# Kernel tuning notes

Measured on AMD Instinct MI355X. Metric: run time of the kernel, lower is better.

The kernel has to match this reference:

```python
import jax, jax.numpy as jnp
import numpy as np


def smooth_l1(x, y):
    d = jnp.abs(x - y)
    return jnp.where(d < 1.0, 0.5 * d * d, d - 0.5)


def setup_inputs() -> dict:
    key = jax.random.key(0)
    k1, k2, k3 = jax.random.split(key, 3)
    B, T, N, D = 4, 28, 1024, 3
    X_v = jax.random.normal(k1, (B, T, N, D), dtype=jnp.float32)
    target_X_v = jax.random.normal(k2, (B, T, N, D), dtype=jnp.float32)
    weights = jax.random.uniform(k3, (B, T), dtype=jnp.float32)
    return {"X_v": X_v, "target_X_v": target_X_v, "weights": weights}


def reference(X_v, target_X_v, weights):
    B = X_v.shape[0]
    # Pairwise squared distances [B,T,N,N] via ||p||^2 + ||t||^2 - 2 p.t
    pn = jnp.sum(X_v * X_v, axis=-1)                 # [B,T,N]
    tn = jnp.sum(target_X_v * target_X_v, axis=-1)   # [B,T,N]
    dist = (pn[..., :, None] + tn[..., None, :]
            - 2.0 * jnp.einsum('btnd,btmd->btnm', X_v, target_X_v))
    minv = jnp.argmin(dist, axis=-1)                 # [B,T,N] int
    # gather nearest target point for each pred point
    tagp = jnp.take_along_axis(target_X_v, minv[..., None], axis=2)  # [B,T,N,3]
    # per-(b,t) mean smooth-L1 over N points x 3 coords
    loss_bt = jnp.mean(smooth_l1(X_v, tagp), axis=(-2, -1))          # [B,T]
    loss = jnp.sum(loss_bt * weights) / B

    prec = jnp.mean(X_v, axis=2)        # [B,T,3]
    tarc = jnp.mean(target_X_v, axis=2) # [B,T,3]
    lossc = jnp.sum(smooth_l1(prec, tarc)) / (B * 3)
    return (loss, lossc)
```

## Files before the change

### kernel.cpp

```cpp
#include <hip/hip_runtime.h>

constexpr int Bc = 4;
constexpr int Tc = 28;
constexpr int Nc = 1024;
constexpr int Dc = 3;
constexpr int BT = Bc * Tc;
constexpr int QT = 256;
constexpr int NQ = 4;

constexpr size_t WS_BESTV = 0;
constexpr size_t WS_BESTI = (size_t)NQ * BT * 256 * 4;
constexpr size_t WS_PSUM  = WS_BESTI + (size_t)NQ * BT * 256 * 4;
constexpr size_t WS_TSUM  = WS_PSUM + BT * 3;

__device__ __forceinline__ float sl1(float d) {
    d = fabsf(d);
    return d < 1.0f ? 0.5f * d * d : d - 0.5f;
}

__global__ __launch_bounds__(256) void chamfer_kernel(
    const float* __restrict__ X, const float* __restrict__ Tg,
    float4* __restrict__ bestvP, int4* __restrict__ bestiP,
    float* __restrict__ psum, float* __restrict__ tsum)
{
    __shared__ float4 sT4[QT];
    __shared__ float sred[4][3];

    const int bt  = blockIdx.x >> 2;
    const int th  = blockIdx.x & 3;
    const int tid = threadIdx.x;

    const float4* x4 = (const float4*)(X + (size_t)bt * (Nc * Dc));
    const float4 a0 = x4[3 * tid + 0];
    const float4 a1 = x4[3 * tid + 1];
    const float4 a2 = x4[3 * tid + 2];

    if (tid < 64) {
        const float4* tg4 = (const float4*)(Tg + (size_t)bt * (Nc * Dc) + th * (QT * 3));
        const float4 r0 = tg4[3 * tid + 0];
        const float4 r1 = tg4[3 * tid + 1];
        const float4 r2 = tg4[3 * tid + 2];
        sT4[4 * tid + 0] = make_float4(r0.x, r0.y, r0.z, fmaf(r0.x, r0.x, fmaf(r0.y, r0.y, r0.z * r0.z)));
        sT4[4 * tid + 1] = make_float4(r0.w, r1.x, r1.y, fmaf(r0.w, r0.w, fmaf(r1.x, r1.x, r1.y * r1.y)));
        sT4[4 * tid + 2] = make_float4(r1.z, r1.w, r2.x, fmaf(r1.z, r1.z, fmaf(r1.w, r1.w, r2.x * r2.x)));
        sT4[4 * tid + 3] = make_float4(r2.y, r2.z, r2.w, fmaf(r2.y, r2.y, fmaf(r2.z, r2.z, r2.w * r2.w)));
        float tx = r0.x + r0.w + r1.z + r2.y;
        float ty = r0.y + r1.x + r1.w + r2.z;
        float tz = r0.z + r1.y + r2.x + r2.w;
        #pragma unroll
        for (int off = 32; off; off >>= 1) {
            tx += __shfl_down(tx, off, 64);
            ty += __shfl_down(ty, off, 64);
            tz += __shfl_down(tz, off, 64);
        }
        if (tid == 0) {
            tsum[(bt * NQ + th) * 3 + 0] = tx;
            tsum[(bt * NQ + th) * 3 + 1] = ty;
            tsum[(bt * NQ + th) * 3 + 2] = tz;
        }
    }
    __syncthreads();

    const float c0[4] = {-2.f * a0.x, -2.f * a0.w, -2.f * a1.z, -2.f * a2.y};
    const float c1[4] = {-2.f * a0.y, -2.f * a1.x, -2.f * a1.w, -2.f * a2.z};
    const float c2[4] = {-2.f * a0.z, -2.f * a1.y, -2.f * a2.x, -2.f * a2.w};

    float best[4] = {3.4e38f, 3.4e38f, 3.4e38f, 3.4e38f};
    int idx[4] = {0, 0, 0, 0};

    constexpr int PF = 4;
    float4 bufA[PF], bufB[PF];
    #pragma unroll
    for (int j = 0; j < PF; ++j) bufA[j] = sT4[j];

    for (int m0 = 0; m0 < QT; m0 += 2 * PF) {
        #pragma unroll
        for (int j = 0; j < PF; ++j) bufB[j] = sT4[m0 + PF + j];
        #pragma unroll
        for (int j = 0; j < PF; ++j) {
            const float4 t = bufA[j];
            const int m = m0 + j;
            #pragma unroll
            for (int k = 0; k < 4; ++k) {
                float v = fmaf(c0[k], t.x, fmaf(c1[k], t.y, fmaf(c2[k], t.z, t.w)));
                bool c = v < best[k]; best[k] = c ? v : best[k]; idx[k] = c ? m : idx[k];
            }
        }
        #pragma unroll
        for (int j = 0; j < PF; ++j) bufA[j] = sT4[(m0 + 2 * PF + j) & (QT - 1)];
        #pragma unroll
        for (int j = 0; j < PF; ++j) {
            const float4 t = bufB[j];
            const int m = m0 + PF + j;
            #pragma unroll
            for (int k = 0; k < 4; ++k) {
                float v = fmaf(c0[k], t.x, fmaf(c1[k], t.y, fmaf(c2[k], t.z, t.w)));
                bool c = v < best[k]; best[k] = c ? v : best[k]; idx[k] = c ? m : idx[k];
            }
        }
    }

    const size_t ob = ((size_t)th * BT + bt) * 256 + tid;
    bestvP[ob] = make_float4(best[0], best[1], best[2], best[3]);
    bestiP[ob] = make_int4(th * QT + idx[0], th * QT + idx[1],
                           th * QT + idx[2], th * QT + idx[3]);

    if (th == 0) {
        float sx = a0.x + a0.w + a1.z + a2.y;
        float sy = a0.y + a1.x + a1.w + a2.z;
        float sz = a0.z + a1.y + a2.x + a2.w;
        const int lane = tid & 63, wid = tid >> 6;
        #pragma unroll
        for (int off = 32; off; off >>= 1) {
            sx += __shfl_down(sx, off, 64);
            sy += __shfl_down(sy, off, 64);
            sz += __shfl_down(sz, off, 64);
        }
        if (lane == 0) { sred[wid][0] = sx; sred[wid][1] = sy; sred[wid][2] = sz; }
        __syncthreads();
        if (tid == 0) {
            #pragma unroll
            for (int k = 0; k < 3; ++k)
                psum[bt * 3 + k] = sred[0][k] + sred[1][k] + sred[2][k] + sred[3][k];
        }
    }
}

__global__ __launch_bounds__(256) void gather_finalize_kernel(
    const float* __restrict__ X, const float* __restrict__ Tg,
    const float* __restrict__ W,
    const float4* __restrict__ bestvP, const int4* __restrict__ bestiP,
    const float* __restrict__ psum, const float* __restrict__ tsum,
    float* __restrict__ out)
{
    __shared__ float sred[4];
    __shared__ float sred2[4];
    const int bt  = blockIdx.x;
    const int tid = threadIdx.x;
    const size_t rb = (size_t)bt * 256 + tid;

    float4 bv = bestvP[rb];
    int4   bi = bestiP[rb];
    float best[4] = {bv.x, bv.y, bv.z, bv.w};
    int   idx[4]  = {bi.x, bi.y, bi.z, bi.w};
    #pragma unroll
    for (int q = 1; q < NQ; ++q) {
        const float4 v2 = bestvP[(size_t)q * BT * 256 + rb];
        const int4   i2 = bestiP[(size_t)q * BT * 256 + rb];
        if (v2.x < best[0]) { best[0] = v2.x; idx[0] = i2.x; }
        if (v2.y < best[1]) { best[1] = v2.y; idx[1] = i2.y; }
        if (v2.z < best[2]) { best[2] = v2.z; idx[2] = i2.z; }
        if (v2.w < best[3]) { best[3] = v2.w; idx[3] = i2.w; }
    }

    const float* tb = Tg + (size_t)bt * (Nc * Dc);
    const float4* x4 = (const float4*)(X + (size_t)bt * (Nc * Dc));
    const float4 a0 = x4[3 * tid + 0];
    const float4 a1 = x4[3 * tid + 1];
    const float4 a2 = x4[3 * tid + 2];
    const float px[4] = {a0.x, a0.w, a1.z, a2.y};
    const float py[4] = {a0.y, a1.x, a1.w, a2.z};
    const float pz[4] = {a0.z, a1.y, a2.x, a2.w};

    float s = 0.0f;
    #pragma unroll
    for (int k = 0; k < 4; ++k) {
        const float tx = tb[idx[k] * 3 + 0];
        const float ty = tb[idx[k] * 3 + 1];
        const float tz = tb[idx[k] * 3 + 2];
        s += sl1(px[k] - tx) + sl1(py[k] - ty) + sl1(pz[k] - tz);
    }

    const int lane = tid & 63, wid = tid >> 6;
    #pragma unroll
    for (int off = 32; off; off >>= 1) s += __shfl_down(s, off, 64);
    if (lane == 0) sred[wid] = s;
    __syncthreads();
    if (tid == 0) {
        float tot = sred[0] + sred[1] + sred[2] + sred[3];
        atomicAdd(out, tot * W[bt] * (1.0f / (Nc * Dc)) * (1.0f / Bc));
    }

    if (bt == 0) {
        float lc = 0.0f;
        if (tid < BT) {
            const float inv = 1.0f / Nc;
            #pragma unroll
            for (int c = 0; c < 3; ++c) {
                float pm = psum[tid * 3 + c] * inv;
                float tm = (tsum[(tid * NQ + 0) * 3 + c] + tsum[(tid * NQ + 1) * 3 + c]
                          + tsum[(tid * NQ + 2) * 3 + c] + tsum[(tid * NQ + 3) * 3 + c]) * inv;
                lc += sl1(pm - tm);
            }
        }
        float v = lc;
        #pragma unroll
        for (int off = 32; off; off >>= 1) v += __shfl_down(v, off, 64);
        if (lane == 0) sred2[wid] = v;
        __syncthreads();
        if (tid == 0) {
            float tlc = sred2[0] + sred2[1] + sred2[2] + sred2[3];
            atomicAdd(out + 1, tlc * (1.0f / (Bc * Dc)));
        }
    }
}

extern "C" void kernel_launch(void* const* d_in, const int* in_sizes, int n_in,
                              void* d_out, int out_size, void* d_ws, size_t ws_size,
                              hipStream_t stream) {
    const float* X  = (const float*)d_in[0];
    const float* Tg = (const float*)d_in[1];
    const float* W  = (const float*)d_in[2];
    float* out = (float*)d_out;
    float* ws  = (float*)d_ws;

    float4* bestvP = (float4*)(ws + WS_BESTV);
    int4*   bestiP = (int4*)(ws + WS_BESTI);
    float*  psum   = ws + WS_PSUM;
    float*  tsum   = ws + WS_TSUM;

    hipMemsetAsync(out, 0, 2 * sizeof(float), stream);
    chamfer_kernel<<<BT * NQ, 256, 0, stream>>>(X, Tg, bestvP, bestiP, psum, tsum);
    gather_finalize_kernel<<<BT, 256, 0, stream>>>(X, Tg, W, bestvP, bestiP, psum, tsum, out);
}
```

Measured before the change: 85.61 us.

## Split targets into 8 chunks, read targets via uniform global loads, move centroid sums

Each (b,t) now has its target set split into 8 chunks of 128 instead of 4 of 256, giving 896 blocks for better CU fill. Target points are read directly from global memory with wave-uniform (scalar-friendly) loads, and their squared norm is recomputed in-loop instead of being staged through shared memory, which removes the LDS fill and the barrier. The centroid sums move into the finalize kernel, which now does a 7-value block reduction and applies the per-bt centroid loss with an atomic. In exchange, the finalize kernel reads twice as many partial results, and each inner step does a few extra FMAs for the norm.

```diff
diff --git a/kernel.cpp b/kernel.cpp
--- a/kernel.cpp
+++ b/kernel.cpp
@@ -5,136 +5,75 @@
 constexpr int Nc = 1024;
 constexpr int Dc = 3;
 constexpr int BT = Bc * Tc;
-constexpr int QT = 256;
-constexpr int NQ = 4;
+constexpr int TQ = 128;
+constexpr int NQ = Nc / TQ;
 
 constexpr size_t WS_BESTV = 0;
 constexpr size_t WS_BESTI = (size_t)NQ * BT * 256 * 4;
-constexpr size_t WS_PSUM  = WS_BESTI + (size_t)NQ * BT * 256 * 4;
-constexpr size_t WS_TSUM  = WS_PSUM + BT * 3;
 
 __device__ __forceinline__ float sl1(float d) {
     d = fabsf(d);
     return d < 1.0f ? 0.5f * d * d : d - 0.5f;
 }
 
-__global__ __launch_bounds__(256) void chamfer_kernel(
+__global__ __launch_bounds__(256, 4) void chamfer_kernel(
     const float* __restrict__ X, const float* __restrict__ Tg,
-    float4* __restrict__ bestvP, int4* __restrict__ bestiP,
-    float* __restrict__ psum, float* __restrict__ tsum)
+    float4* __restrict__ bestvP, int4* __restrict__ bestiP)
 {
-    __shared__ float4 sT4[QT];
-    __shared__ float sred[4][3];
-
-    const int bt  = blockIdx.x >> 2;
-    const int th  = blockIdx.x & 3;
+    const int bt  = blockIdx.x >> 3;
+    const int th  = blockIdx.x & 7;
     const int tid = threadIdx.x;
 
     const float4* x4 = (const float4*)(X + (size_t)bt * (Nc * Dc));
     const float4 a0 = x4[3 * tid + 0];
     const float4 a1 = x4[3 * tid + 1];
     const float4 a2 = x4[3 * tid + 2];
+    const float cx[4] = {-2.f * a0.x, -2.f * a0.w, -2.f * a1.z, -2.f * a2.y};
+    const float cy[4] = {-2.f * a0.y, -2.f * a1.x, -2.f * a1.w, -2.f * a2.z};
+    const float cz[4] = {-2.f * a0.z, -2.f * a1.y, -2.f * a2.x, -2.f * a2.w};
 
-    if (tid < 64) {
-        const float4* tg4 = (const float4*)(Tg + (size_t)bt * (Nc * Dc) + th * (QT * 3));
-        const float4 r0 = tg4[3 * tid + 0];
-        const float4 r1 = tg4[3 * tid + 1];
-        const float4 r2 = tg4[3 * tid + 2];
-        sT4[4 * tid + 0] = make_float4(r0.x, r0.y, r0.z, fmaf(r0.x, r0.x, fmaf(r0.y, r0.y, r0.z * r0.z)));
-        sT4[4 * tid + 1] = make_float4(r0.w, r1.x, r1.y, fmaf(r0.w, r0.w, fmaf(r1.x, r1.x, r1.y * r1.y)));
-        sT4[4 * tid + 2] = make_float4(r1.z, r1.w, r2.x, fmaf(r1.z, r1.z, fmaf(r1.w, r1.w, r2.x * r2.x)));
-        sT4[4 * tid + 3] = make_float4(r2.y, r2.z, r2.w, fmaf(r2.y, r2.y, fmaf(r2.z, r2.z, r2.w * r2.w)));
-        float tx = r0.x + r0.w + r1.z + r2.y;
-        float ty = r0.y + r1.x + r1.w + r2.z;
-        float tz = r0.z + r1.y + r2.x + r2.w;
-        #pragma unroll
-        for (int off = 32; off; off >>= 1) {
-            tx += __shfl_down(tx, off, 64);
-            ty += __shfl_down(ty, off, 64);
-            tz += __shfl_down(tz, off, 64);
-        }
-        if (tid == 0) {
-            tsum[(bt * NQ + th) * 3 + 0] = tx;
-            tsum[(bt * NQ + th) * 3 + 1] = ty;
-            tsum[(bt * NQ + th) * 3 + 2] = tz;
-        }
-    }
-    __syncthreads();
-
-    const float c0[4] = {-2.f * a0.x, -2.f * a0.w, -2.f * a1.z, -2.f * a2.y};
-    const float c1[4] = {-2.f * a0.y, -2.f * a1.x, -2.f * a1.w, -2.f * a2.z};
-    const float c2[4] = {-2.f * a0.z, -2.f * a1.y, -2.f * a2.x, -2.f * a2.w};
+    const float* __restrict__ tq = Tg + (size_t)bt * (Nc * Dc) + th * (TQ * 3);
 
     float best[4] = {3.4e38f, 3.4e38f, 3.4e38f, 3.4e38f};
     int idx[4] = {0, 0, 0, 0};
 
-    constexpr int PF = 4;
-    float4 bufA[PF], bufB[PF];
-    #pragma unroll
-    for (int j = 0; j < PF; ++j) bufA[j] = sT4[j];
-
-    for (int m0 = 0; m0 < QT; m0 += 2 * PF) {
+    constexpr int G = 8;
+    for (int m0 = 0; m0 < TQ; m0 += G) {
+        float t[G][3];
         #pragma unroll
-        for (int j = 0; j < PF; ++j) bufB[j] = sT4[m0 + PF + j];
+        for (int j = 0; j < G; ++j) {
+            t[j][0] = tq[3 * (m0 + j) + 0];
+            t[j][1] = tq[3 * (m0 + j) + 1];
+            t[j][2] = tq[3 * (m0 + j) + 2];
+        }
         #pragma unroll
-        for (int j = 0; j < PF; ++j) {
-            const float4 t = bufA[j];
+        for (int j = 0; j < G; ++j) {
+            const float tx = t[j][0], ty = t[j][1], tz = t[j][2];
+            const float tn = fmaf(tx, tx, fmaf(ty, ty, tz * tz));
             const int m = m0 + j;
             #pragma unroll
             for (int k = 0; k < 4; ++k) {
-                float v = fmaf(c0[k], t.x, fmaf(c1[k], t.y, fmaf(c2[k], t.z, t.w)));
-                bool c = v < best[k]; best[k] = c ? v : best[k]; idx[k] = c ? m : idx[k];
-            }
-        }
-        #pragma unroll
-        for (int j = 0; j < PF; ++j) bufA[j] = sT4[(m0 + 2 * PF + j) & (QT - 1)];
-        #pragma unroll
-        for (int j = 0; j < PF; ++j) {
-            const float4 t = bufB[j];
-            const int m = m0 + PF + j;
-            #pragma unroll
-            for (int k = 0; k < 4; ++k) {
-                float v = fmaf(c0[k], t.x, fmaf(c1[k], t.y, fmaf(c2[k], t.z, t.w)));
-                bool c = v < best[k]; best[k] = c ? v : best[k]; idx[k] = c ? m : idx[k];
+                float v = fmaf(cx[k], tx, fmaf(cy[k], ty, fmaf(cz[k], tz, tn)));
+                bool c = v < best[k];
+                best[k] = c ? v : best[k];
+                idx[k]  = c ? m : idx[k];
             }
         }
     }
 
     const size_t ob = ((size_t)th * BT + bt) * 256 + tid;
     bestvP[ob] = make_float4(best[0], best[1], best[2], best[3]);
-    bestiP[ob] = make_int4(th * QT + idx[0], th * QT + idx[1],
-                           th * QT + idx[2], th * QT + idx[3]);
-
-    if (th == 0) {
-        float sx = a0.x + a0.w + a1.z + a2.y;
-        float sy = a0.y + a1.x + a1.w + a2.z;
-        float sz = a0.z + a1.y + a2.x + a2.w;
-        const int lane = tid & 63, wid = tid >> 6;
-        #pragma unroll
-        for (int off = 32; off; off >>= 1) {
-            sx += __shfl_down(sx, off, 64);
-            sy += __shfl_down(sy, off, 64);
-            sz += __shfl_down(sz, off, 64);
-        }
-        if (lane == 0) { sred[wid][0] = sx; sred[wid][1] = sy; sred[wid][2] = sz; }
-        __syncthreads();
-        if (tid == 0) {
-            #pragma unroll
-            for (int k = 0; k < 3; ++k)
-                psum[bt * 3 + k] = sred[0][k] + sred[1][k] + sred[2][k] + sred[3][k];
-        }
-    }
+    bestiP[ob] = make_int4(th * TQ + idx[0], th * TQ + idx[1],
+                           th * TQ + idx[2], th * TQ + idx[3]);
 }
 
 __global__ __launch_bounds__(256) void gather_finalize_kernel(
     const float* __restrict__ X, const float* __restrict__ Tg,
     const float* __restrict__ W,
     const float4* __restrict__ bestvP, const int4* __restrict__ bestiP,
-    const float* __restrict__ psum, const float* __restrict__ tsum,
     float* __restrict__ out)
 {
-    __shared__ float sred[4];
-    __shared__ float sred2[4];
+    __shared__ float sred[4][8];
     const int bt  = blockIdx.x;
     const int tid = threadIdx.x;
     const size_t rb = (size_t)bt * 256 + tid;
@@ -153,7 +92,6 @@
         if (v2.w < best[3]) { best[3] = v2.w; idx[3] = i2.w; }
     }
 
-    const float* tb = Tg + (size_t)bt * (Nc * Dc);
     const float4* x4 = (const float4*)(X + (size_t)bt * (Nc * Dc));
     const float4 a0 = x4[3 * tid + 0];
     const float4 a1 = x4[3 * tid + 1];
@@ -162,6 +100,12 @@
     const float py[4] = {a0.y, a1.x, a1.w, a2.z};
     const float pz[4] = {a0.z, a1.y, a2.x, a2.w};
 
+    const float4* t4 = (const float4*)(Tg + (size_t)bt * (Nc * Dc));
+    const float4 r0 = t4[3 * tid + 0];
+    const float4 r1 = t4[3 * tid + 1];
+    const float4 r2 = t4[3 * tid + 2];
+
+    const float* tb = Tg + (size_t)bt * (Nc * Dc);
     float s = 0.0f;
     #pragma unroll
     for (int k = 0; k < 4; ++k) {
@@ -171,37 +115,35 @@
         s += sl1(px[k] - tx) + sl1(py[k] - ty) + sl1(pz[k] - tz);
     }
 
+    float vals[7] = {
+        s,
+        px[0] + px[1] + px[2] + px[3],
+        py[0] + py[1] + py[2] + py[3],
+        pz[0] + pz[1] + pz[2] + pz[3],
+        r0.x + r0.w + r1.z + r2.y,
+        r0.y + r1.x + r1.w + r2.z,
+        r0.z + r1.y + r2.x + r2.w
+    };
     const int lane = tid & 63, wid = tid >> 6;
     #pragma unroll
-    for (int off = 32; off; off >>= 1) s += __shfl_down(s, off, 64);
-    if (lane == 0) sred[wid] = s;
+    for (int k = 0; k < 7; ++k) {
+        float v = vals[k];
+        #pragma unroll
+        for (int off = 32; off; off >>= 1) v += __shfl_down(v, off, 64);
+        if (lane == 0) sred[wid][k] = v;
+    }
     __syncthreads();
     if (tid == 0) {
-        float tot = sred[0] + sred[1] + sred[2] + sred[3];
-        atomicAdd(out, tot * W[bt] * (1.0f / (Nc * Dc)) * (1.0f / Bc));
-    }
-
-    if (bt == 0) {
-        float lc = 0.0f;
-        if (tid < BT) {
-            const float inv = 1.0f / Nc;
-            #pragma unroll
-            for (int c = 0; c < 3; ++c) {
-                float pm = psum[tid * 3 + c] * inv;
-                float tm = (tsum[(tid * NQ + 0) * 3 + c] + tsum[(tid * NQ + 1) * 3 + c]
-                          + tsum[(tid * NQ + 2) * 3 + c] + tsum[(tid * NQ + 3) * 3 + c]) * inv;
-                lc += sl1(pm - tm);
-            }
-        }
-        float v = lc;
+        float tot[7];
         #pragma unroll
-        for (int off = 32; off; off >>= 1) v += __shfl_down(v, off, 64);
-        if (lane == 0) sred2[wid] = v;
-        __syncthreads();
-        if (tid == 0) {
-            float tlc = sred2[0] + sred2[1] + sred2[2] + sred2[3];
-            atomicAdd(out + 1, tlc * (1.0f / (Bc * Dc)));
-        }
+        for (int k = 0; k < 7; ++k)
+            tot[k] = sred[0][k] + sred[1][k] + sred[2][k] + sred[3][k];
+        atomicAdd(out, tot[0] * W[bt] * (1.0f / (Nc * Dc)) * (1.0f / Bc));
+        const float inv = 1.0f / Nc;
+        float lc = sl1((tot[1] - tot[4]) * inv)
+                 + sl1((tot[2] - tot[5]) * inv)
+                 + sl1((tot[3] - tot[6]) * inv);
+        atomicAdd(out + 1, lc * (1.0f / (Bc * Dc)));
     }
 }
 
@@ -216,10 +158,8 @@
 
     float4* bestvP = (float4*)(ws + WS_BESTV);
     int4*   bestiP = (int4*)(ws + WS_BESTI);
-    float*  psum   = ws + WS_PSUM;
-    float*  tsum   = ws + WS_TSUM;
 
     hipMemsetAsync(out, 0, 2 * sizeof(float), stream);
-    chamfer_kernel<<<BT * NQ, 256, 0, stream>>>(X, Tg, bestvP, bestiP, psum, tsum);
-    gather_finalize_kernel<<<BT, 256, 0, stream>>>(X, Tg, W, bestvP, bestiP, psum, tsum, out);
+    chamfer_kernel<<<BT * NQ, 256, 0, stream>>>(X, Tg, bestvP, bestiP);
+    gather_finalize_kernel<<<BT, 256, 0, stream>>>(X, Tg, W, bestvP, bestiP, out);
 }
```

Result: slower. 93.87 us (+9.6%).
